# Kernel tuning notes

Hardware: AMD Instinct MI355X
Metric: run time of the kernel (lower is better)

Reference implementation:

```python
import jax, jax.numpy as jnp
import numpy as np

H = 256    # hidden_size
CVQ = 64   # vq_ph_channel
K = 128    # vq_ph_codebook_dim
NL = 5     # num_layers per ConvBlocks
NB = 2     # layers_in_block
KS = 3     # kernel_size


def _ln_c(x, g, b, eps=1e-5):
    # LayerNorm over channel dim of a [B, C, T] tensor
    m = jnp.mean(x, axis=1, keepdims=True)
    v = jnp.mean((x - m) ** 2, axis=1, keepdims=True)
    return (x - m) * jax.lax.rsqrt(v + eps) * g[None, :, None] + b[None, :, None]


def _causal_conv(x, w, b):
    # x [B,Cin,T], w [Cout,Cin,K]; left (causal) padding of K-1
    y = jax.lax.conv_general_dilated(x, w, (1,), [(w.shape[-1] - 1, 0)],
                                     dimension_numbers=('NCH', 'OIH', 'NCH'))
    return y + b[None, :, None]


def _pw(x, w, b):
    # pointwise (kernel-size-1) conv: w [Cout, Cin]
    return jnp.einsum('oi,bit->bot', w, x) + b[None, :, None]


def _conv_blocks(x, mask, ln_g, ln_b, w1, b1, w2, b2, last_g, last_b, post_w, post_b):
    # LeftPadConvBlocks: NL residual blocks x NB sub-blocks of
    # LN -> causal conv (C->2C, k=3) -> *k^-0.5 -> GELU -> 1x1 conv (2C->C), residual + mask
    scale = KS ** -0.5
    for i in range(NL):
        for j in range(NB):
            h = _ln_c(x, ln_g[i, j], ln_b[i, j])
            h = _causal_conv(h, w1[i, j], b1[i, j]) * scale
            h = jax.nn.gelu(h, approximate=False)
            h = _pw(h, w2[i, j], b2[i, j])
            x = (x + h) * mask
    x = _ln_c(x, last_g, last_b) * mask
    x = _causal_conv(x, post_w, post_b) * mask
    return x


def _group_by_segs(h_bct, mel2ph, L):
    # scatter-mean mel frames into phoneme segments; index 0 = padding (dropped)
    h = jnp.swapaxes(h_bct, 1, 2)  # [B, T, H]
    def one(hb, mb):
        s = jnp.zeros((L + 1, hb.shape[-1]), hb.dtype).at[mb].add(hb)
        c = jnp.zeros((L + 1,), hb.dtype).at[mb].add(1.0)
        return s[1:] / jnp.clip(c[1:], 1.0)[:, None]
    g = jax.vmap(one)(h, mel2ph)   # [B, L, H]
    return jnp.swapaxes(g, 1, 2)   # [B, H, L]


def _vq(z, codebook, beta=0.25):
    # EMA-VQ forward math: nearest-codebook lookup + straight-through + commitment loss
    x = jnp.swapaxes(z, 1, 2)                                # [B, T, C]
    d = (jnp.sum(x ** 2, -1, keepdims=True)
         - 2.0 * jnp.einsum('btc,kc->btk', x, codebook)
         + jnp.sum(codebook ** 2, -1))                       # [B, T, K]
    idx = jnp.argmin(d, axis=-1)                             # [B, T]
    q = codebook[idx]                                        # [B, T, C]
    loss = beta * jnp.mean((x - jax.lax.stop_gradient(q)) ** 2)
    q_st = x + jax.lax.stop_gradient(q - x)
    return jnp.swapaxes(q_st, 1, 2), loss, idx


def setup_inputs() -> dict:
    key = jax.random.key(0)
    ks = list(jax.random.split(key, 64))
    it = iter(ks)
    B, T, L = 16, 2048, 512
    f = lambda shape, s: jax.random.normal(next(it), shape, jnp.float32) * s
    inp = {}
    inp['x'] = jax.random.normal(next(it), (B, 80, T), jnp.float32)
    inp['in_nonpadding'] = jnp.ones((B, 1, T), jnp.float32)
    inp['in_mel2ph'] = jnp.sort(jax.random.randint(next(it), (B, T), 1, L + 1), axis=-1)
    inp['ph_nonpadding'] = jnp.ones((B, 1, L), jnp.float32)
    inp['conv_in_w'] = f((H, 80), 0.05)
    inp['conv_in_b'] = jnp.zeros((H,), jnp.float32)
    for p in ('enc', 'pn'):
        inp[p + '_ln_g'] = jnp.ones((NL, NB, H), jnp.float32)
        inp[p + '_ln_b'] = jnp.zeros((NL, NB, H), jnp.float32)
        inp[p + '_w1'] = f((NL, NB, 2 * H, H, KS), 0.03)
        inp[p + '_b1'] = jnp.zeros((NL, NB, 2 * H), jnp.float32)
        inp[p + '_w2'] = f((NL, NB, H, 2 * H), 0.03)
        inp[p + '_b2'] = jnp.zeros((NL, NB, H), jnp.float32)
        inp[p + '_last_g'] = jnp.ones((H,), jnp.float32)
        inp[p + '_last_b'] = jnp.zeros((H,), jnp.float32)
        inp[p + '_post_w'] = f((H, H, KS), 0.03)
        inp[p + '_post_b'] = jnp.zeros((H,), jnp.float32)
    inp['proj_in_w'] = f((CVQ, H), 0.05)
    inp['proj_in_b'] = jnp.zeros((CVQ,), jnp.float32)
    inp['proj_out_w'] = f((H, CVQ), 0.05)
    inp['proj_out_b'] = jnp.zeros((H,), jnp.float32)
    inp['codebook'] = f((K, CVQ), 0.1)
    return inp


def reference(x, in_nonpadding, in_mel2ph, ph_nonpadding,
              conv_in_w, conv_in_b,
              enc_ln_g, enc_ln_b, enc_w1, enc_b1, enc_w2, enc_b2,
              enc_last_g, enc_last_b, enc_post_w, enc_post_b,
              pn_ln_g, pn_ln_b, pn_w1, pn_b1, pn_w2, pn_b2,
              pn_last_g, pn_last_b, pn_post_w, pn_post_b,
              proj_in_w, proj_in_b, proj_out_w, proj_out_b, codebook):
    L = ph_nonpadding.shape[-1]
    h = _pw(x, conv_in_w, conv_in_b) * in_nonpadding                     # ph_conv_in
    h = _conv_blocks(h, in_nonpadding, enc_ln_g, enc_ln_b, enc_w1, enc_b1,
                     enc_w2, enc_b2, enc_last_g, enc_last_b,
                     enc_post_w, enc_post_b) * in_nonpadding             # ph_encoder
    h = _group_by_segs(h, in_mel2ph, L)                                  # [B, H, L]
    h = _conv_blocks(h, ph_nonpadding, pn_ln_g, pn_ln_b, pn_w1, pn_b1,
                     pn_w2, pn_b2, pn_last_g, pn_last_b,
                     pn_post_w, pn_post_b) * ph_nonpadding               # ph_postnet
    z = _pw(h, proj_in_w, proj_in_b)                                     # ph_latents_proj_in
    q, vq_loss, idx = _vq(z, codebook)                                   # VQ
    out = _pw(q, proj_out_w, proj_out_b)                                 # ph_latents_proj_out
    return out, vq_loss, idx
```

## Files before the change

### kernel.cpp

```cpp
#include <hip/hip_runtime.h>
#include <hip/hip_bf16.h>


typedef unsigned short u16;
typedef unsigned int u32;
typedef __attribute__((ext_vector_type(8))) _Float16 f16x8;
typedef __attribute__((ext_vector_type(16))) float f32x16;

#define OUT_LOSS_OFF 2097152
#define OUT_IDX_OFF  2097153

__device__ __forceinline__ void split_f16(float x, u16& h, u16& l) {
    union { _Float16 f; u16 u; } a, b;
    a.f = (_Float16)x;
    float hf = (float)a.f;
    b.f = (_Float16)(x - hf);
    h = a.u; l = b.u;
}

__global__ __launch_bounds__(256) void k_t_mat(const float* __restrict__ w,
                                               float* __restrict__ wt,
                                               int G, int O, int I) {
    size_t n = (size_t)G * O * I;
    for (size_t i = (size_t)blockIdx.x * 256 + threadIdx.x; i < n;
         i += (size_t)gridDim.x * 256) {
        int ci = (int)(i % I);
        int o  = (int)((i / I) % O);
        int g  = (int)(i / ((size_t)I * O));
        wt[((size_t)g * I + ci) * O + o] = w[i];
    }
}

__global__ __launch_bounds__(256) void k_t_w1mf(const float* __restrict__ w,
                                                u16* __restrict__ BH,
                                                u16* __restrict__ BL, int S) {
    size_t N = (size_t)S * 3 * 16 * 16 * 64 * 8;
    for (size_t i = (size_t)blockIdx.x * 256 + threadIdx.x; i < N;
         i += (size_t)gridDim.x * 256) {
        int j = (int)(i & 7); size_t r = i >> 3;
        int L = (int)(r & 63); r >>= 6;
        int nt = (int)(r & 15); r >>= 4;
        int kb = (int)(r & 15); r >>= 4;
        int k3 = (int)(r % 3); int s = (int)(r / 3);
        int oc = nt * 32 + (L & 31);
        int c = kb * 16 + ((L >> 5) << 3) + j;
        float v = w[(((size_t)s * 512 + oc) * 256 + c) * 3 + k3];
        u16 h, l; split_f16(v, h, l);
        BH[i] = h; BL[i] = l;
    }
}

__global__ __launch_bounds__(256) void k_t_w2mf(const float* __restrict__ w,
                                                u16* __restrict__ BH,
                                                u16* __restrict__ BL, int S) {
    size_t N = (size_t)S * 32 * 8 * 64 * 8;
    for (size_t i = (size_t)blockIdx.x * 256 + threadIdx.x; i < N;
         i += (size_t)gridDim.x * 256) {
        int j = (int)(i & 7);
        int L = (int)((i >> 3) & 63);
        int nt = (int)((i >> 9) & 7);
        int kb = (int)((i >> 12) & 31);
        int s = (int)(i >> 17);
        int oc = nt * 32 + (L & 31);
        int ic = kb * 16 + ((L >> 5) << 3) + j;
        float v = w[((size_t)s * 256 + oc) * 512 + ic];
        u16 h, l; split_f16(v, h, l);
        BH[i] = h; BL[i] = l;
    }
}

__global__ __launch_bounds__(256) void k_t_wpmf(const float* __restrict__ w,
                                                u16* __restrict__ BH,
                                                u16* __restrict__ BL) {
    int i = blockIdx.x * 256 + threadIdx.x;
    int j = i & 7;
    int L = (i >> 3) & 63;
    int nt = (i >> 9) & 7;
    int kb = (i >> 12) & 15;
    int k3 = i >> 16;
    int oc = nt * 32 + (L & 31);
    int c = kb * 16 + ((L >> 5) << 3) + j;
    float v = w[((size_t)oc * 256 + c) * 3 + k3];
    u16 h, l; split_f16(v, h, l);
    BH[i] = h; BL[i] = l;
}

template <int CIN, int COUT, int CHUNK, bool STATS>
__global__ __launch_bounds__(256) void k_pw(const float* __restrict__ x,
                                            const float* __restrict__ wt,
                                            const float* __restrict__ bias,
                                            const float* __restrict__ mask,
                                            float* __restrict__ y,
                                            float* __restrict__ MM,
                                            float* __restrict__ IV, int T) {
    extern __shared__ float X[];
    constexpr int NG = COUT / CHUNK;
    __shared__ float rs[64 * NG], rs2[64 * NG];
    const int b = blockIdx.y, t0 = blockIdx.x * 64;
    for (int i = threadIdx.x; i < CIN * 64; i += 256) {
        int ci = i >> 6, j = i & 63;
        X[i] = x[((size_t)b * CIN + ci) * T + t0 + j];
    }
    __syncthreads();
    const int tl = threadIdx.x & 63;
    const int g = __builtin_amdgcn_readfirstlane((int)(threadIdx.x >> 6));
    float acc[CHUNK];
#pragma unroll
    for (int o = 0; o < CHUNK; o++) acc[o] = 0.f;
    for (int i = 0; i < CIN; i++) {
        float xv = X[i * 64 + tl];
        const float* wr = wt + (size_t)i * COUT + g * CHUNK;
#pragma unroll
        for (int o = 0; o < CHUNK; o++) acc[o] = fmaf(wr[o], xv, acc[o]);
    }
    float mk = mask ? mask[(size_t)b * T + t0 + tl] : 1.0f;
    float s = 0.f, s2 = 0.f;
#pragma unroll
    for (int o = 0; o < CHUNK; o++) {
        int oc = g * CHUNK + o;
        float val = (acc[o] + bias[oc]) * mk;
        y[((size_t)b * COUT + oc) * T + t0 + tl] = val;
        s += val; s2 += val * val;
    }
    if constexpr (STATS) {
        rs[g * 64 + tl] = s; rs2[g * 64 + tl] = s2;
        __syncthreads();
        if (threadIdx.x < 64) {
            float ss = 0.f, ss2 = 0.f;
#pragma unroll
            for (int gg = 0; gg < NG; gg++) {
                ss += rs[gg * 64 + threadIdx.x];
                ss2 += rs2[gg * 64 + threadIdx.x];
            }
            float m = ss * (1.0f / COUT);
            float var = ss2 * (1.0f / COUT) - m * m;
            MM[(size_t)b * T + t0 + threadIdx.x] = m;
            IV[(size_t)b * T + t0 + threadIdx.x] = 1.0f / sqrtf(var + 1e-5f);
        }
    }
}

__global__ __launch_bounds__(512, 6) void k_sub(
    const float* __restrict__ xin, float* __restrict__ xout,
    const float* __restrict__ MMi, const float* __restrict__ IVi,
    const float* __restrict__ lng, const float* __restrict__ lnb,
    const u16* __restrict__ B1H, const u16* __restrict__ B1L,
    const float* __restrict__ b1,
    const u16* __restrict__ B2H, const u16* __restrict__ B2L,
    const float* __restrict__ b2, const float* __restrict__ mask,
    float* __restrict__ MMo, float* __restrict__ IVo, int T) {
    __shared__ __align__(16) char smem[40128];
    u16* LH = (u16*)smem;
    u16* LL = (u16*)(smem + 17952);
    u16* GH = (u16*)smem;
    u16* GL = (u16*)(smem + 17952);
    float* SOUT = (float*)smem;
    float* rs  = (float*)(smem + 36032);
    float* rs2 = (float*)(smem + 38080);

    const int tid = threadIdx.x;
    const int b = blockIdx.y, t0 = blockIdx.x * 32;
    const size_t xoff = (size_t)b * 256 * T;
    const size_t bT = (size_t)b * T;

    {
        int jj = tid & 31;
        int cg = tid >> 5;
        int t = t0 - 2 + jj;
        bool ok = (t >= 0);
        float m = ok ? MMi[bT + t] : 0.f;
        float v = ok ? IVi[bT + t] : 0.f;
#pragma unroll
        for (int i = 0; i < 16; i++) {
            int c = cg + i * 16;
            float xv = ok ? xin[xoff + (size_t)c * T + t] : 0.f;
            float ln = ok ? ((xv - m) * v * lng[c] + lnb[c]) : 0.f;
            u16 h, l; split_f16(ln, h, l);
            LH[jj * 264 + c] = h; LL[jj * 264 + c] = l;
        }
        int j2 = 32 + (tid >> 8);
        int c2 = tid & 255;
        int t2 = t0 + 30 + (tid >> 8);
        float m2 = MMi[bT + t2], v2 = IVi[bT + t2];
        float x2 = xin[xoff + (size_t)c2 * T + t2];
        float ln2 = (x2 - m2) * v2 * lng[c2] + lnb[c2];
        u16 h2, l2; split_f16(ln2, h2, l2);
        LH[j2 * 264 + c2] = h2; LL[j2 * 264 + c2] = l2;
    }
    __syncthreads();

    const int lane = tid & 63;
    const int w = tid >> 6;
    const int arow = lane & 31;
    const int acol = (lane >> 5) << 3;
    const int thalf = (lane >> 5) << 2;
    const float ks = 0.5773502691896258f;
    const int oc_l = w * 32 + (lane & 31);
    const u16* b1h0 = B1H + (size_t)w * 512 + (size_t)lane * 8;
    const u16* b1l0 = B1L + (size_t)w * 512 + (size_t)lane * 8;
    const u16* b1h1 = B1H + (size_t)(8 + w) * 512 + (size_t)lane * 8;
    const u16* b1l1 = B1L + (size_t)(8 + w) * 512 + (size_t)lane * 8;
    const u16* b2h = B2H + (size_t)w * 512 + (size_t)lane * 8;
    const u16* b2l = B2L + (size_t)w * 512 + (size_t)lane * 8;
    const int grow = (lane & 31) * 264;

    f32x16 c0, c1;
#pragma unroll
    for (int r = 0; r < 16; r++) { c0[r] = 0.f; c1[r] = 0.f; }
    __builtin_amdgcn_s_setprio(1);
#pragma unroll 4
    for (int kk = 0; kk < 48; kk++) {
        int k3 = kk >> 4, kb = kk & 15;
        int ao = (arow + k3) * 264 + kb * 16 + acol;
        f16x8 ah = *(const f16x8*)&LH[ao];
        f16x8 al = *(const f16x8*)&LL[ao];
        f16x8 bh0 = *(const f16x8*)(b1h0 + (size_t)kk * 8192);
        f16x8 bl0 = *(const f16x8*)(b1l0 + (size_t)kk * 8192);
        f16x8 bh1 = *(const f16x8*)(b1h1 + (size_t)kk * 8192);
        f16x8 bl1 = *(const f16x8*)(b1l1 + (size_t)kk * 8192);
        c0 = __builtin_amdgcn_mfma_f32_32x32x16_f16(ah, bh0, c0, 0, 0, 0);
        c1 = __builtin_amdgcn_mfma_f32_32x32x16_f16(ah, bh1, c1, 0, 0, 0);
        c0 = __builtin_amdgcn_mfma_f32_32x32x16_f16(ah, bl0, c0, 0, 0, 0);
        c1 = __builtin_amdgcn_mfma_f32_32x32x16_f16(ah, bl1, c1, 0, 0, 0);
        c0 = __builtin_amdgcn_mfma_f32_32x32x16_f16(al, bh0, c0, 0, 0, 0);
        c1 = __builtin_amdgcn_mfma_f32_32x32x16_f16(al, bh1, c1, 0, 0, 0);
    }
    __builtin_amdgcn_s_setprio(0);
    __syncthreads();

    {
        float bb = b1[oc_l];
#pragma unroll
        for (int r = 0; r < 16; r++) {
            int trow = thalf + ((r >> 2) << 3) + (r & 3);
            float y = (c0[r] + bb) * ks;
            float ge = 0.5f * y * (1.0f + erff(y * 0.7071067811865476f));
            u16 h, l; split_f16(ge, h, l);
            GH[trow * 264 + oc_l] = h; GL[trow * 264 + oc_l] = l;
        }
    }
    __syncthreads();

    f32x16 c2acc;
#pragma unroll
    for (int r = 0; r < 16; r++) c2acc[r] = 0.f;
    __builtin_amdgcn_s_setprio(1);
#pragma unroll 4
    for (int i = 0; i < 16; i++) {
        f16x8 gh = *(const f16x8*)&GH[grow + i * 16 + acol];
        f16x8 gl = *(const f16x8*)&GL[grow + i * 16 + acol];
        f16x8 bh2 = *(const f16x8*)(b2h + (size_t)i * 4096);
        f16x8 bl2 = *(const f16x8*)(b2l + (size_t)i * 4096);
        c2acc = __builtin_amdgcn_mfma_f32_32x32x16_f16(gh, bh2, c2acc, 0, 0, 0);
        c2acc = __builtin_amdgcn_mfma_f32_32x32x16_f16(gh, bl2, c2acc, 0, 0, 0);
        c2acc = __builtin_amdgcn_mfma_f32_32x32x16_f16(gl, bh2, c2acc, 0, 0, 0);
    }
    __builtin_amdgcn_s_setprio(0);
    __syncthreads();

    {
        float bb = b1[256 + oc_l];
#pragma unroll
        for (int r = 0; r < 16; r++) {
            int trow = thalf + ((r >> 2) << 3) + (r & 3);
            float y = (c1[r] + bb) * ks;
            float ge = 0.5f * y * (1.0f + erff(y * 0.7071067811865476f));
            u16 h, l; split_f16(ge, h, l);
            GH[trow * 264 + oc_l] = h; GL[trow * 264 + oc_l] = l;
        }
    }
    __syncthreads();

    __builtin_amdgcn_s_setprio(1);
#pragma unroll 4
    for (int i = 0; i < 16; i++) {
        f16x8 gh = *(const f16x8*)&GH[grow + i * 16 + acol];
        f16x8 gl = *(const f16x8*)&GL[grow + i * 16 + acol];
        f16x8 bh2 = *(const f16x8*)(b2h + (size_t)(16 + i) * 4096);
        f16x8 bl2 = *(const f16x8*)(b2l + (size_t)(16 + i) * 4096);
        c2acc = __builtin_amdgcn_mfma_f32_32x32x16_f16(gh, bh2, c2acc, 0, 0, 0);
        c2acc = __builtin_amdgcn_mfma_f32_32x32x16_f16(gh, bl2, c2acc, 0, 0, 0);
        c2acc = __builtin_amdgcn_mfma_f32_32x32x16_f16(gl, bh2, c2acc, 0, 0, 0);
    }
    __builtin_amdgcn_s_setprio(0);
    __syncthreads();

#pragma unroll
    for (int r = 0; r < 16; r++) {
        int trow = thalf + ((r >> 2) << 3) + (r & 3);
        SOUT[trow * 260 + oc_l] = c2acc[r];
    }
    __syncthreads();
    {
        int t = tid & 31, cg = tid >> 5;
        float mk = mask[bT + t0 + t];
        float s = 0.f, s2 = 0.f;
#pragma unroll
        for (int i = 0; i < 16; i++) {
            int c = cg * 16 + i;
            size_t adr = xoff + (size_t)c * T + t0 + t;
            float val = (xin[adr] + SOUT[t * 260 + c] + b2[c]) * mk;
            xout[adr] = val;
            s += val; s2 += val * val;
        }
        rs[tid] = s; rs2[tid] = s2;
    }
    __syncthreads();
    if (tid < 32) {
        float ss = 0.f, ss2 = 0.f;
#pragma unroll
        for (int k = 0; k < 16; k++) {
            ss += rs[k * 32 + tid]; ss2 += rs2[k * 32 + tid];
        }
        float m = ss * (1.0f / 256.0f);
        float var = ss2 * (1.0f / 256.0f) - m * m;
        MMo[bT + t0 + tid] = m;
        IVo[bT + t0 + tid] = 1.0f / sqrtf(var + 1e-5f);
    }
}

__global__ __launch_bounds__(512, 8) void k_lnc(
    const float* __restrict__ xin, float* __restrict__ xout,
    const float* __restrict__ MM, const float* __restrict__ IV,
    const float* __restrict__ lg, const float* __restrict__ lb,
    const u16* __restrict__ BH, const u16* __restrict__ BL,
    const float* __restrict__ bias, const float* __restrict__ mask, int T) {
    __shared__ __align__(16) char smem[35904];
    u16* LH = (u16*)smem;
    u16* LL = (u16*)(smem + 17952);
    float* SOUT = (float*)smem;

    const int tid = threadIdx.x;
    const int b = blockIdx.y, t0 = blockIdx.x * 32;
    const size_t xoff = (size_t)b * 256 * T;
    const size_t bT = (size_t)b * T;

    {
        int jj = tid & 31;
        int cg = tid >> 5;
        int t = t0 - 2 + jj;
        bool ok = (t >= 0);
        float m = ok ? MM[bT + t] : 0.f;
        float v = ok ? IV[bT + t] : 0.f;
        float mk = ok ? mask[bT + t] : 0.f;
#pragma unroll
        for (int i = 0; i < 16; i++) {
            int c = cg + i * 16;
            float xv = ok ? xin[xoff + (size_t)c * T + t] : 0.f;
            float ln = ok ? ((xv - m) * v * lg[c] + lb[c]) * mk : 0.f;
            u16 h, l; split_f16(ln, h, l);
            LH[jj * 264 + c] = h; LL[jj * 264 + c] = l;
        }
        int j2 = 32 + (tid >> 8);
        int c2 = tid & 255;
        int t2 = t0 + 30 + (tid >> 8);
        float ln2 = ((xin[xoff + (size_t)c2 * T + t2] - MM[bT + t2]) *
                     IV[bT + t2] * lg[c2] + lb[c2]) * mask[bT + t2];
        u16 h2, l2; split_f16(ln2, h2, l2);
        LH[j2 * 264 + c2] = h2; LL[j2 * 264 + c2] = l2;
    }
    __syncthreads();

    const int lane = tid & 63;
    const int w = tid >> 6;
    const int arow = lane & 31;
    const int acol = (lane >> 5) << 3;
    const int thalf = (lane >> 5) << 2;
    const u16* bph = BH + (size_t)w * 512 + (size_t)lane * 8;
    const u16* bpl = BL + (size_t)w * 512 + (size_t)lane * 8;

    f32x16 aH, aM;
#pragma unroll
    for (int r = 0; r < 16; r++) { aH[r] = 0.f; aM[r] = 0.f; }
    __builtin_amdgcn_s_setprio(1);
#pragma unroll 4
    for (int kk = 0; kk < 48; kk++) {
        int k3 = kk >> 4, kb = kk & 15;
        int ao = (arow + k3) * 264 + kb * 16 + acol;
        f16x8 ah = *(const f16x8*)&LH[ao];
        f16x8 al = *(const f16x8*)&LL[ao];
        f16x8 bh = *(const f16x8*)(bph + (size_t)kk * 4096);
        f16x8 bl = *(const f16x8*)(bpl + (size_t)kk * 4096);
        aH = __builtin_amdgcn_mfma_f32_32x32x16_f16(ah, bh, aH, 0, 0, 0);
        aM = __builtin_amdgcn_mfma_f32_32x32x16_f16(ah, bl, aM, 0, 0, 0);
        aM = __builtin_amdgcn_mfma_f32_32x32x16_f16(al, bh, aM, 0, 0, 0);
    }
    __builtin_amdgcn_s_setprio(0);
    __syncthreads();
    {
        int oc = w * 32 + (lane & 31);
#pragma unroll
        for (int r = 0; r < 16; r++) {
            int trow = thalf + ((r >> 2) << 3) + (r & 3);
            SOUT[trow * 260 + oc] = aH[r] + aM[r];
        }
    }
    __syncthreads();
    {
        int t = tid & 31, cg = tid >> 5;
        float mk = mask[bT + t0 + t];
#pragma unroll
        for (int i = 0; i < 16; i++) {
            int c = cg * 16 + i;
            xout[xoff + (size_t)c * T + t0 + t] =
                (SOUT[t * 260 + c] + bias[c]) * mk;
        }
    }
}

__global__ __launch_bounds__(256) void k_counts(const int* __restrict__ m2p,
                                                int* __restrict__ cnt) {
    __shared__ int c[512];
    int b = blockIdx.x;
    for (int i = threadIdx.x; i < 512; i += 256) c[i] = 0;
    __syncthreads();
    for (int t = threadIdx.x; t < 2048; t += 256) {
        int p = m2p[b * 2048 + t];
        if (p >= 1 && p <= 512) atomicAdd(&c[p - 1], 1);
    }
    __syncthreads();
    for (int i = threadIdx.x; i < 512; i += 256) cnt[b * 512 + i] = c[i];
}

__global__ __launch_bounds__(256) void k_scatter(const float* __restrict__ h,
                                                 const int* __restrict__ m2p,
                                                 float* __restrict__ g) {
    extern __shared__ float sm[];
    float* HT = sm;
    int* ph = (int*)(sm + 256 * 65);
    int b = blockIdx.y, t0 = blockIdx.x * 64;
    if (threadIdx.x < 64) ph[threadIdx.x] = m2p[b * 2048 + t0 + threadIdx.x];
    for (int i = threadIdx.x; i < 256 * 64; i += 256) {
        int c = i >> 6, j = i & 63;
        HT[c * 65 + j] = h[((size_t)b * 256 + c) * 2048 + t0 + j];
    }
    __syncthreads();
    int c = threadIdx.x;
    float run = 0.f;
    int cur = ph[0];
    for (int j = 0; j < 64; j++) {
        int p = ph[j];
        if (p != cur) {
            if (cur >= 1 && cur <= 512)
                atomicAdd(&g[((size_t)b * 256 + c) * 512 + cur - 1], run);
            run = 0.f;
            cur = p;
        }
        run += HT[c * 65 + j];
    }
    if (cur >= 1 && cur <= 512)
        atomicAdd(&g[((size_t)b * 256 + c) * 512 + cur - 1], run);
}

__global__ __launch_bounds__(512) void k_postprep(float* __restrict__ g,
                                                  const int* __restrict__ cnt,
                                                  float* __restrict__ MM,
                                                  float* __restrict__ IV) {
    int b = blockIdx.x, l = threadIdx.x;
    int c1 = cnt[b * 512 + l];
    if (c1 < 1) c1 = 1;
    float rc = 1.0f / (float)c1;
    float s = 0.f, s2 = 0.f;
    for (int c = 0; c < 256; c++) {
        size_t idx = ((size_t)b * 256 + c) * 512 + l;
        float v = g[idx] * rc;
        g[idx] = v;
        s += v; s2 += v * v;
    }
    float m = s * (1.0f / 256.0f);
    float var = s2 * (1.0f / 256.0f) - m * m;
    MM[(size_t)b * 512 + l] = m;
    IV[(size_t)b * 512 + l] = 1.0f / sqrtf(var + 1e-5f);
}

__global__ __launch_bounds__(256) void k_vq(const float* __restrict__ z,
                                            const float* __restrict__ cb,
                                            int* __restrict__ idxout,
                                            float* __restrict__ out,
                                            float* __restrict__ lossacc) {
    int n = blockIdx.x * 256 + threadIdx.x;
    int b = n >> 9, l = n & 511;
    float zr[64];
#pragma unroll
    for (int c = 0; c < 64; c++) zr[c] = z[((size_t)b * 64 + c) * 512 + l];
    float best = 3.4e38f;
    int bi = 0;
    for (int k = 0; k < 128; k++) {
        const float* cr = cb + k * 64;
        float d = 0.f;
#pragma unroll
        for (int c = 0; c < 64; c++) {
            float t = zr[c] - cr[c];
            d = fmaf(t, t, d);
        }
        if (d < best) { best = d; bi = k; }
    }
    idxout[n] = bi;
    out[OUT_IDX_OFF + n] = (float)bi;
    atomicAdd(lossacc, best);
}

__global__ void k_loss(const float* __restrict__ acc, float* __restrict__ out) {
    if (threadIdx.x == 0 && blockIdx.x == 0)
        out[OUT_LOSS_OFF] = 0.25f * acc[0] * (1.0f / 524288.0f);
}

__global__ __launch_bounds__(256) void k_projout(const float* __restrict__ cb,
                                                 const int* __restrict__ idx,
                                                 const float* __restrict__ wt,
                                                 const float* __restrict__ bias,
                                                 float* __restrict__ out) {
    __shared__ float Q[64 * 64];
    __shared__ int ids[64];
    int b = blockIdx.y, l0 = blockIdx.x * 64;
    if (threadIdx.x < 64) ids[threadIdx.x] = idx[b * 512 + l0 + threadIdx.x];
    __syncthreads();
    for (int i = threadIdx.x; i < 4096; i += 256) {
        int c = i >> 6, l = i & 63;
        Q[c * 64 + l] = cb[ids[l] * 64 + c];
    }
    __syncthreads();
    int tl = threadIdx.x & 63;
    int g = __builtin_amdgcn_readfirstlane((int)(threadIdx.x >> 6));
    float acc[64];
#pragma unroll
    for (int o = 0; o < 64; o++) acc[o] = 0.f;
    for (int i = 0; i < 64; i++) {
        float xv = Q[i * 64 + tl];
        const float* wr = wt + i * 256 + g * 64;
#pragma unroll
        for (int o = 0; o < 64; o++) acc[o] = fmaf(wr[o], xv, acc[o]);
    }
#pragma unroll
    for (int o = 0; o < 64; o++) {
        int oc = g * 64 + o;
        out[(size_t)b * 131072 + (size_t)oc * 512 + l0 + tl] = acc[o] + bias[oc];
    }
}

extern "C" void kernel_launch(void* const* d_in, const int* in_sizes, int n_in,
                              void* d_out, int out_size, void* d_ws, size_t ws_size,
                              hipStream_t stream) {
    (void)in_sizes; (void)n_in; (void)out_size; (void)ws_size;
    const float* x          = (const float*)d_in[0];
    const float* in_np      = (const float*)d_in[1];
    const int*   mel2ph     = (const int*)d_in[2];
    const float* ph_np      = (const float*)d_in[3];
    const float* conv_in_w  = (const float*)d_in[4];
    const float* conv_in_b  = (const float*)d_in[5];
    const float* e_ln_g = (const float*)d_in[6];
    const float* e_ln_b = (const float*)d_in[7];
    const float* e_w1   = (const float*)d_in[8];
    const float* e_b1   = (const float*)d_in[9];
    const float* e_w2   = (const float*)d_in[10];
    const float* e_b2   = (const float*)d_in[11];
    const float* e_lg   = (const float*)d_in[12];
    const float* e_lb   = (const float*)d_in[13];
    const float* e_pw   = (const float*)d_in[14];
    const float* e_pb   = (const float*)d_in[15];
    const float* p_ln_g = (const float*)d_in[16];
    const float* p_ln_b = (const float*)d_in[17];
    const float* p_w1   = (const float*)d_in[18];
    const float* p_b1   = (const float*)d_in[19];
    const float* p_w2   = (const float*)d_in[20];
    const float* p_b2   = (const float*)d_in[21];
    const float* p_lg   = (const float*)d_in[22];
    const float* p_lb   = (const float*)d_in[23];
    const float* p_pw   = (const float*)d_in[24];
    const float* p_pb   = (const float*)d_in[25];
    const float* proj_in_w  = (const float*)d_in[26];
    const float* proj_in_b  = (const float*)d_in[27];
    const float* proj_out_w = (const float*)d_in[28];
    const float* proj_out_b = (const float*)d_in[29];
    const float* codebook   = (const float*)d_in[30];
    float* out = (float*)d_out;

    float* ws = (float*)d_ws;
    float* A      = ws;
    float* Bb     = A + 8388608;
    float* CINT   = Bb + 8388608;
    float* PINT   = CINT + 20480;
    float* POUTT  = PINT + 16384;
    float* Z      = POUTT + 16384;
    float* MM0    = Z + 524288;
    float* IV0    = MM0 + 32768;
    float* MM1    = IV0 + 32768;
    float* IV1    = MM1 + 32768;
    int*   CNT    = (int*)(IV1 + 32768);
    int*   IDX    = CNT + 8192;
    float* LOSS   = (float*)(IDX + 8192);
    u16*   BH1E   = (u16*)(LOSS + 64);
    u16*   BL1E   = BH1E + 3932160;
    u16*   BH1P   = BL1E + 3932160;
    u16*   BL1P   = BH1P + 3932160;
    u16*   BH2E   = BL1P + 3932160;
    u16*   BL2E   = BH2E + 1310720;
    u16*   BH2P   = BL2E + 1310720;
    u16*   BL2P   = BH2P + 1310720;
    u16*   PH_E   = BL2P + 1310720;
    u16*   PL_E   = PH_E + 196608;
    u16*   PH_P   = PL_E + 196608;
    u16*   PL_P   = PH_P + 196608;

    k_t_w1mf<<<dim3(4096), dim3(256), 0, stream>>>(e_w1, BH1E, BL1E, 10);
    k_t_w1mf<<<dim3(4096), dim3(256), 0, stream>>>(p_w1, BH1P, BL1P, 10);
    k_t_w2mf<<<dim3(2048), dim3(256), 0, stream>>>(e_w2, BH2E, BL2E, 10);
    k_t_w2mf<<<dim3(2048), dim3(256), 0, stream>>>(p_w2, BH2P, BL2P, 10);
    k_t_wpmf<<<dim3(768),  dim3(256), 0, stream>>>(e_pw, PH_E, PL_E);
    k_t_wpmf<<<dim3(768),  dim3(256), 0, stream>>>(p_pw, PH_P, PL_P);
    k_t_mat  <<<dim3(80),  dim3(256), 0, stream>>>(conv_in_w, CINT, 1, 256, 80);
    k_t_mat  <<<dim3(64),  dim3(256), 0, stream>>>(proj_in_w, PINT, 1, 64, 256);
    k_t_mat  <<<dim3(64),  dim3(256), 0, stream>>>(proj_out_w, POUTT, 1, 256, 64);

    const size_t sm_scat = 256 * 65 * sizeof(float) + 64 * sizeof(int);

    k_pw<80, 256, 64, true><<<dim3(32, 16), dim3(256), 80 * 64 * 4, stream>>>(
        x, CINT, conv_in_b, in_np, A, MM0, IV0, 2048);

    float* cur = A;
    float* nxt = Bb;
    for (int s = 0; s < 10; s++) {
        float* mi = (s & 1) ? MM1 : MM0;
        float* vi = (s & 1) ? IV1 : IV0;
        float* mo = (s & 1) ? MM0 : MM1;
        float* vo = (s & 1) ? IV0 : IV1;
        k_sub<<<dim3(64, 16), dim3(512), 0, stream>>>(
            cur, nxt, mi, vi, e_ln_g + s * 256, e_ln_b + s * 256,
            BH1E + (size_t)s * 393216, BL1E + (size_t)s * 393216, e_b1 + s * 512,
            BH2E + (size_t)s * 131072, BL2E + (size_t)s * 131072, e_b2 + s * 256,
            in_np, mo, vo, 2048);
        float* t = cur; cur = nxt; nxt = t;
    }
    k_lnc<<<dim3(64, 16), dim3(512), 0, stream>>>(
        cur, nxt, MM0, IV0, e_lg, e_lb, PH_E, PL_E, e_pb, in_np, 2048);

    hipMemsetAsync(A, 0, (size_t)2097152 * 4, stream);
    hipMemsetAsync(LOSS, 0, 4, stream);
    k_counts<<<dim3(16), dim3(256), 0, stream>>>(mel2ph, CNT);
    k_scatter<<<dim3(32, 16), dim3(256), sm_scat, stream>>>(Bb, mel2ph, A);
    k_postprep<<<dim3(16), dim3(512), 0, stream>>>(A, CNT, MM0, IV0);

    cur = A; nxt = Bb;
    for (int s = 0; s < 10; s++) {
        float* mi = (s & 1) ? MM1 : MM0;
        float* vi = (s & 1) ? IV1 : IV0;
        float* mo = (s & 1) ? MM0 : MM1;
        float* vo = (s & 1) ? IV0 : IV1;
        k_sub<<<dim3(16, 16), dim3(512), 0, stream>>>(
            cur, nxt, mi, vi, p_ln_g + s * 256, p_ln_b + s * 256,
            BH1P + (size_t)s * 393216, BL1P + (size_t)s * 393216, p_b1 + s * 512,
            BH2P + (size_t)s * 131072, BL2P + (size_t)s * 131072, p_b2 + s * 256,
            ph_np, mo, vo, 512);
        float* t = cur; cur = nxt; nxt = t;
    }
    k_lnc<<<dim3(16, 16), dim3(512), 0, stream>>>(
        cur, nxt, MM0, IV0, p_lg, p_lb, PH_P, PL_P, p_pb, ph_np, 512);

    k_pw<256, 64, 16, false><<<dim3(8, 16), dim3(256), 256 * 64 * 4, stream>>>(
        Bb, PINT, proj_in_b, nullptr, Z, nullptr, nullptr, 512);

    k_vq<<<dim3(32), dim3(256), 0, stream>>>(Z, codebook, IDX, out, LOSS);
    k_loss<<<dim3(1), dim3(64), 0, stream>>>(LOSS, out);
    k_projout<<<dim3(8, 16), dim3(256), 0, stream>>>(codebook, IDX, POUTT,
                                                     proj_out_b, out);
}
```

Before: 2.416 ms.

## Template conv sub-block kernels on time tile and use 64-frame tiles for encoder

```diff
diff --git a/kernel.cpp b/kernel.cpp
--- a/kernel.cpp
+++ b/kernel.cpp
@@ -140,7 +140,8 @@
     }
 }
 
-__global__ __launch_bounds__(512, 6) void k_sub(
+template <int M>
+__global__ __launch_bounds__(512, (M == 32 ? 6 : 4)) void k_sub(
     const float* __restrict__ xin, float* __restrict__ xout,
     const float* __restrict__ MMi, const float* __restrict__ IVi,
     const float* __restrict__ lng, const float* __restrict__ lnb,
@@ -149,38 +150,42 @@
     const u16* __restrict__ B2H, const u16* __restrict__ B2L,
     const float* __restrict__ b2, const float* __restrict__ mask,
     float* __restrict__ MMo, float* __restrict__ IVo, int T) {
-    __shared__ __align__(16) char smem[40128];
+    constexpr int MT = M / 32;
+    constexpr int SH = (M + 2) * 264 * 2;
+    constexpr int CG = 512 / M;
+    constexpr int CPT = 256 / CG;
+    __shared__ __align__(16) char smem[2 * SH + 4096];
     u16* LH = (u16*)smem;
-    u16* LL = (u16*)(smem + 17952);
+    u16* LL = (u16*)(smem + SH);
     u16* GH = (u16*)smem;
-    u16* GL = (u16*)(smem + 17952);
+    u16* GL = (u16*)(smem + SH);
     float* SOUT = (float*)smem;
-    float* rs  = (float*)(smem + 36032);
-    float* rs2 = (float*)(smem + 38080);
+    float* rs  = (float*)(smem + 2 * SH);
+    float* rs2 = (float*)(smem + 2 * SH + 2048);
 
     const int tid = threadIdx.x;
-    const int b = blockIdx.y, t0 = blockIdx.x * 32;
+    const int b = blockIdx.y, t0 = blockIdx.x * M;
     const size_t xoff = (size_t)b * 256 * T;
     const size_t bT = (size_t)b * T;
 
     {
-        int jj = tid & 31;
-        int cg = tid >> 5;
+        int jj = tid & (M - 1);
+        int cg = tid / M;
         int t = t0 - 2 + jj;
         bool ok = (t >= 0);
         float m = ok ? MMi[bT + t] : 0.f;
         float v = ok ? IVi[bT + t] : 0.f;
 #pragma unroll
-        for (int i = 0; i < 16; i++) {
-            int c = cg + i * 16;
+        for (int i = 0; i < CPT; i++) {
+            int c = cg + i * CG;
             float xv = ok ? xin[xoff + (size_t)c * T + t] : 0.f;
             float ln = ok ? ((xv - m) * v * lng[c] + lnb[c]) : 0.f;
             u16 h, l; split_f16(ln, h, l);
             LH[jj * 264 + c] = h; LL[jj * 264 + c] = l;
         }
-        int j2 = 32 + (tid >> 8);
+        int j2 = M + (tid >> 8);
         int c2 = tid & 255;
-        int t2 = t0 + 30 + (tid >> 8);
+        int t2 = t0 + (M - 2) + (tid >> 8);
         float m2 = MMi[bT + t2], v2 = IVi[bT + t2];
         float x2 = xin[xoff + (size_t)c2 * T + t2];
         float ln2 = (x2 - m2) * v2 * lng[c2] + lnb[c2];
@@ -202,28 +207,32 @@
     const u16* b1l1 = B1L + (size_t)(8 + w) * 512 + (size_t)lane * 8;
     const u16* b2h = B2H + (size_t)w * 512 + (size_t)lane * 8;
     const u16* b2l = B2L + (size_t)w * 512 + (size_t)lane * 8;
-    const int grow = (lane & 31) * 264;
-
-    f32x16 c0, c1;
-#pragma unroll
-    for (int r = 0; r < 16; r++) { c0[r] = 0.f; c1[r] = 0.f; }
+
+    f32x16 c0[MT], c1[MT];
+#pragma unroll
+    for (int m = 0; m < MT; m++)
+#pragma unroll
+        for (int r = 0; r < 16; r++) { c0[m][r] = 0.f; c1[m][r] = 0.f; }
     __builtin_amdgcn_s_setprio(1);
-#pragma unroll 4
+#pragma unroll 2
     for (int kk = 0; kk < 48; kk++) {
         int k3 = kk >> 4, kb = kk & 15;
-        int ao = (arow + k3) * 264 + kb * 16 + acol;
-        f16x8 ah = *(const f16x8*)&LH[ao];
-        f16x8 al = *(const f16x8*)&LL[ao];
         f16x8 bh0 = *(const f16x8*)(b1h0 + (size_t)kk * 8192);
         f16x8 bl0 = *(const f16x8*)(b1l0 + (size_t)kk * 8192);
         f16x8 bh1 = *(const f16x8*)(b1h1 + (size_t)kk * 8192);
         f16x8 bl1 = *(const f16x8*)(b1l1 + (size_t)kk * 8192);
-        c0 = __builtin_amdgcn_mfma_f32_32x32x16_f16(ah, bh0, c0, 0, 0, 0);
-        c1 = __builtin_amdgcn_mfma_f32_32x32x16_f16(ah, bh1, c1, 0, 0, 0);
-        c0 = __builtin_amdgcn_mfma_f32_32x32x16_f16(ah, bl0, c0, 0, 0, 0);
-        c1 = __builtin_amdgcn_mfma_f32_32x32x16_f16(ah, bl1, c1, 0, 0, 0);
-        c0 = __builtin_amdgcn_mfma_f32_32x32x16_f16(al, bh0, c0, 0, 0, 0);
-        c1 = __builtin_amdgcn_mfma_f32_32x32x16_f16(al, bh1, c1, 0, 0, 0);
+#pragma unroll
+        for (int m = 0; m < MT; m++) {
+            int ao = (m * 32 + arow + k3) * 264 + kb * 16 + acol;
+            f16x8 ah = *(const f16x8*)&LH[ao];
+            f16x8 al = *(const f16x8*)&LL[ao];
+            c0[m] = __builtin_amdgcn_mfma_f32_32x32x16_f16(ah, bh0, c0[m], 0, 0, 0);
+            c1[m] = __builtin_amdgcn_mfma_f32_32x32x16_f16(ah, bh1, c1[m], 0, 0, 0);
+            c0[m] = __builtin_amdgcn_mfma_f32_32x32x16_f16(ah, bl0, c0[m], 0, 0, 0);
+            c1[m] = __builtin_amdgcn_mfma_f32_32x32x16_f16(ah, bl1, c1[m], 0, 0, 0);
+            c0[m] = __builtin_amdgcn_mfma_f32_32x32x16_f16(al, bh0, c0[m], 0, 0, 0);
+            c1[m] = __builtin_amdgcn_mfma_f32_32x32x16_f16(al, bh1, c1[m], 0, 0, 0);
+        }
     }
     __builtin_amdgcn_s_setprio(0);
     __syncthreads();
@@ -231,29 +240,37 @@
     {
         float bb = b1[oc_l];
 #pragma unroll
-        for (int r = 0; r < 16; r++) {
-            int trow = thalf + ((r >> 2) << 3) + (r & 3);
-            float y = (c0[r] + bb) * ks;
-            float ge = 0.5f * y * (1.0f + erff(y * 0.7071067811865476f));
-            u16 h, l; split_f16(ge, h, l);
-            GH[trow * 264 + oc_l] = h; GL[trow * 264 + oc_l] = l;
-        }
-    }
-    __syncthreads();
-
-    f32x16 c2acc;
-#pragma unroll
-    for (int r = 0; r < 16; r++) c2acc[r] = 0.f;
+        for (int m = 0; m < MT; m++)
+#pragma unroll
+            for (int r = 0; r < 16; r++) {
+                int trow = m * 32 + thalf + ((r >> 2) << 3) + (r & 3);
+                float y = (c0[m][r] + bb) * ks;
+                float ge = 0.5f * y * (1.0f + erff(y * 0.7071067811865476f));
+                u16 h, l; split_f16(ge, h, l);
+                GH[trow * 264 + oc_l] = h; GL[trow * 264 + oc_l] = l;
+            }
+    }
+    __syncthreads();
+
+    f32x16 c2acc[MT];
+#pragma unroll
+    for (int m = 0; m < MT; m++)
+#pragma unroll
+        for (int r = 0; r < 16; r++) c2acc[m][r] = 0.f;
     __builtin_amdgcn_s_setprio(1);
-#pragma unroll 4
+#pragma unroll 2
     for (int i = 0; i < 16; i++) {
-        f16x8 gh = *(const f16x8*)&GH[grow + i * 16 + acol];
-        f16x8 gl = *(const f16x8*)&GL[grow + i * 16 + acol];
         f16x8 bh2 = *(const f16x8*)(b2h + (size_t)i * 4096);
         f16x8 bl2 = *(const f16x8*)(b2l + (size_t)i * 4096);
-        c2acc = __builtin_amdgcn_mfma_f32_32x32x16_f16(gh, bh2, c2acc, 0, 0, 0);
-        c2acc = __builtin_amdgcn_mfma_f32_32x32x16_f16(gh, bl2, c2acc, 0, 0, 0);
-        c2acc = __builtin_amdgcn_mfma_f32_32x32x16_f16(gl, bh2, c2acc, 0, 0, 0);
+#pragma unroll
+        for (int m = 0; m < MT; m++) {
+            int go = (m * 32 + arow) * 264 + i * 16 + acol;
+            f16x8 gh = *(const f16x8*)&GH[go];
+            f16x8 gl = *(const f16x8*)&GL[go];
+            c2acc[m] = __builtin_amdgcn_mfma_f32_32x32x16_f16(gh, bh2, c2acc[m], 0, 0, 0);
+            c2acc[m] = __builtin_amdgcn_mfma_f32_32x32x16_f16(gh, bl2, c2acc[m], 0, 0, 0);
+            c2acc[m] = __builtin_amdgcn_mfma_f32_32x32x16_f16(gl, bh2, c2acc[m], 0, 0, 0);
+        }
     }
     __builtin_amdgcn_s_setprio(0);
     __syncthreads();
@@ -261,43 +278,51 @@
     {
         float bb = b1[256 + oc_l];
 #pragma unroll
-        for (int r = 0; r < 16; r++) {
-            int trow = thalf + ((r >> 2) << 3) + (r & 3);
-            float y = (c1[r] + bb) * ks;
-            float ge = 0.5f * y * (1.0f + erff(y * 0.7071067811865476f));
-            u16 h, l; split_f16(ge, h, l);
-            GH[trow * 264 + oc_l] = h; GL[trow * 264 + oc_l] = l;
-        }
+        for (int m = 0; m < MT; m++)
+#pragma unroll
+            for (int r = 0; r < 16; r++) {
+                int trow = m * 32 + thalf + ((r >> 2) << 3) + (r & 3);
+                float y = (c1[m][r] + bb) * ks;
+                float ge = 0.5f * y * (1.0f + erff(y * 0.7071067811865476f));
+                u16 h, l; split_f16(ge, h, l);
+                GH[trow * 264 + oc_l] = h; GL[trow * 264 + oc_l] = l;
+            }
     }
     __syncthreads();
 
     __builtin_amdgcn_s_setprio(1);
-#pragma unroll 4
+#pragma unroll 2
     for (int i = 0; i < 16; i++) {
-        f16x8 gh = *(const f16x8*)&GH[grow + i * 16 + acol];
-        f16x8 gl = *(const f16x8*)&GL[grow + i * 16 + acol];
         f16x8 bh2 = *(const f16x8*)(b2h + (size_t)(16 + i) * 4096);
         f16x8 bl2 = *(const f16x8*)(b2l + (size_t)(16 + i) * 4096);
-        c2acc = __builtin_amdgcn_mfma_f32_32x32x16_f16(gh, bh2, c2acc, 0, 0, 0);
-        c2acc = __builtin_amdgcn_mfma_f32_32x32x16_f16(gh, bl2, c2acc, 0, 0, 0);
-        c2acc = __builtin_amdgcn_mfma_f32_32x32x16_f16(gl, bh2, c2acc, 0, 0, 0);
+#pragma unroll
+        for (int m = 0; m < MT; m++) {
+            int go = (m * 32 + arow) * 264 + i * 16 + acol;
+            f16x8 gh = *(const f16x8*)&GH[go];
+            f16x8 gl = *(const f16x8*)&GL[go];
+            c2acc[m] = __builtin_amdgcn_mfma_f32_32x32x16_f16(gh, bh2, c2acc[m], 0, 0, 0);
+            c2acc[m] = __builtin_amdgcn_mfma_f32_32x32x16_f16(gh, bl2, c2acc[m], 0, 0, 0);
+            c2acc[m] = __builtin_amdgcn_mfma_f32_32x32x16_f16(gl, bh2, c2acc[m], 0, 0, 0);
+        }
     }
     __builtin_amdgcn_s_setprio(0);
     __syncthreads();
 
 #pragma unroll
-    for (int r = 0; r < 16; r++) {
-        int trow = thalf + ((r >> 2) << 3) + (r & 3);
-        SOUT[trow * 260 + oc_l] = c2acc[r];
-    }
+    for (int m = 0; m < MT; m++)
+#pragma unroll
+        for (int r = 0; r < 16; r++) {
+            int trow = m * 32 + thalf + ((r >> 2) << 3) + (r & 3);
+            SOUT[trow * 260 + oc_l] = c2acc[m][r];
+        }
     __syncthreads();
     {
-        int t = tid & 31, cg = tid >> 5;
+        int t = tid & (M - 1), cg = tid / M;
         float mk = mask[bT + t0 + t];
         float s = 0.f, s2 = 0.f;
 #pragma unroll
-        for (int i = 0; i < 16; i++) {
-            int c = cg * 16 + i;
+        for (int i = 0; i < CPT; i++) {
+            int c = cg * CPT + i;
             size_t adr = xoff + (size_t)c * T + t0 + t;
             float val = (xin[adr] + SOUT[t * 260 + c] + b2[c]) * mk;
             xout[adr] = val;
@@ -306,11 +331,11 @@
         rs[tid] = s; rs2[tid] = s2;
     }
     __syncthreads();
-    if (tid < 32) {
+    if (tid < M) {
         float ss = 0.f, ss2 = 0.f;
 #pragma unroll
-        for (int k = 0; k < 16; k++) {
-            ss += rs[k * 32 + tid]; ss2 += rs2[k * 32 + tid];
+        for (int k = 0; k < CG; k++) {
+            ss += rs[k * M + tid]; ss2 += rs2[k * M + tid];
         }
         float m = ss * (1.0f / 256.0f);
         float var = ss2 * (1.0f / 256.0f) - m * m;
@@ -319,41 +344,46 @@
     }
 }
 
-__global__ __launch_bounds__(512, 8) void k_lnc(
+template <int M>
+__global__ __launch_bounds__(512, (M == 32 ? 8 : 4)) void k_lnc(
     const float* __restrict__ xin, float* __restrict__ xout,
     const float* __restrict__ MM, const float* __restrict__ IV,
     const float* __restrict__ lg, const float* __restrict__ lb,
     const u16* __restrict__ BH, const u16* __restrict__ BL,
     const float* __restrict__ bias, const float* __restrict__ mask, int T) {
-    __shared__ __align__(16) char smem[35904];
+    constexpr int MT = M / 32;
+    constexpr int SH = (M + 2) * 264 * 2;
+    constexpr int CG = 512 / M;
+    constexpr int CPT = 256 / CG;
+    __shared__ __align__(16) char smem[2 * SH];
     u16* LH = (u16*)smem;
-    u16* LL = (u16*)(smem + 17952);
+    u16* LL = (u16*)(smem + SH);
     float* SOUT = (float*)smem;
 
     const int tid = threadIdx.x;
-    const int b = blockIdx.y, t0 = blockIdx.x * 32;
+    const int b = blockIdx.y, t0 = blockIdx.x * M;
     const size_t xoff = (size_t)b * 256 * T;
     const size_t bT = (size_t)b * T;
 
     {
-        int jj = tid & 31;
-        int cg = tid >> 5;
+        int jj = tid & (M - 1);
+        int cg = tid / M;
         int t = t0 - 2 + jj;
         bool ok = (t >= 0);
         float m = ok ? MM[bT + t] : 0.f;
         float v = ok ? IV[bT + t] : 0.f;
         float mk = ok ? mask[bT + t] : 0.f;
 #pragma unroll
-        for (int i = 0; i < 16; i++) {
-            int c = cg + i * 16;
+        for (int i = 0; i < CPT; i++) {
+            int c = cg + i * CG;
             float xv = ok ? xin[xoff + (size_t)c * T + t] : 0.f;
             float ln = ok ? ((xv - m) * v * lg[c] + lb[c]) * mk : 0.f;
             u16 h, l; split_f16(ln, h, l);
             LH[jj * 264 + c] = h; LL[jj * 264 + c] = l;
         }
-        int j2 = 32 + (tid >> 8);
+        int j2 = M + (tid >> 8);
         int c2 = tid & 255;
-        int t2 = t0 + 30 + (tid >> 8);
+        int t2 = t0 + (M - 2) + (tid >> 8);
         float ln2 = ((xin[xoff + (size_t)c2 * T + t2] - MM[bT + t2]) *
                      IV[bT + t2] * lg[c2] + lb[c2]) * mask[bT + t2];
         u16 h2, l2; split_f16(ln2, h2, l2);
@@ -369,39 +399,46 @@
     const u16* bph = BH + (size_t)w * 512 + (size_t)lane * 8;
     const u16* bpl = BL + (size_t)w * 512 + (size_t)lane * 8;
 
-    f32x16 aH, aM;
-#pragma unroll
-    for (int r = 0; r < 16; r++) { aH[r] = 0.f; aM[r] = 0.f; }
+    f32x16 aH[MT], aM[MT];
+#pragma unroll
+    for (int m = 0; m < MT; m++)
+#pragma unroll
+        for (int r = 0; r < 16; r++) { aH[m][r] = 0.f; aM[m][r] = 0.f; }
     __builtin_amdgcn_s_setprio(1);
-#pragma unroll 4
+#pragma unroll 2
     for (int kk = 0; kk < 48; kk++) {
         int k3 = kk >> 4, kb = kk & 15;
-        int ao = (arow + k3) * 264 + kb * 16 + acol;
-        f16x8 ah = *(const f16x8*)&LH[ao];
-        f16x8 al = *(const f16x8*)&LL[ao];
         f16x8 bh = *(const f16x8*)(bph + (size_t)kk * 4096);
         f16x8 bl = *(const f16x8*)(bpl + (size_t)kk * 4096);
-        aH = __builtin_amdgcn_mfma_f32_32x32x16_f16(ah, bh, aH, 0, 0, 0);
-        aM = __builtin_amdgcn_mfma_f32_32x32x16_f16(ah, bl, aM, 0, 0, 0);
-        aM = __builtin_amdgcn_mfma_f32_32x32x16_f16(al, bh, aM, 0, 0, 0);
+#pragma unroll
+        for (int m = 0; m < MT; m++) {
+            int ao = (m * 32 + arow + k3) * 264 + kb * 16 + acol;
+            f16x8 ah = *(const f16x8*)&LH[ao];
+            f16x8 al = *(const f16x8*)&LL[ao];
+            aH[m] = __builtin_amdgcn_mfma_f32_32x32x16_f16(ah, bh, aH[m], 0, 0, 0);
+            aM[m] = __builtin_amdgcn_mfma_f32_32x32x16_f16(ah, bl, aM[m], 0, 0, 0);
+            aM[m] = __builtin_amdgcn_mfma_f32_32x32x16_f16(al, bh, aM[m], 0, 0, 0);
+        }
     }
     __builtin_amdgcn_s_setprio(0);
     __syncthreads();
     {
         int oc = w * 32 + (lane & 31);
 #pragma unroll
-        for (int r = 0; r < 16; r++) {
-            int trow = thalf + ((r >> 2) << 3) + (r & 3);
-            SOUT[trow * 260 + oc] = aH[r] + aM[r];
-        }
+        for (int m = 0; m < MT; m++)
+#pragma unroll
+            for (int r = 0; r < 16; r++) {
+                int trow = m * 32 + thalf + ((r >> 2) << 3) + (r & 3);
+                SOUT[trow * 260 + oc] = aH[m][r] + aM[m][r];
+            }
     }
     __syncthreads();
     {
-        int t = tid & 31, cg = tid >> 5;
+        int t = tid & (M - 1), cg = tid / M;
         float mk = mask[bT + t0 + t];
 #pragma unroll
-        for (int i = 0; i < 16; i++) {
-            int c = cg * 16 + i;
+        for (int i = 0; i < CPT; i++) {
+            int c = cg * CPT + i;
             xout[xoff + (size_t)c * T + t0 + t] =
                 (SOUT[t * 260 + c] + bias[c]) * mk;
         }
@@ -624,14 +661,14 @@
         float* vi = (s & 1) ? IV1 : IV0;
         float* mo = (s & 1) ? MM0 : MM1;
         float* vo = (s & 1) ? IV0 : IV1;
-        k_sub<<<dim3(64, 16), dim3(512), 0, stream>>>(
+        k_sub<64><<<dim3(32, 16), dim3(512), 0, stream>>>(
             cur, nxt, mi, vi, e_ln_g + s * 256, e_ln_b + s * 256,
             BH1E + (size_t)s * 393216, BL1E + (size_t)s * 393216, e_b1 + s * 512,
             BH2E + (size_t)s * 131072, BL2E + (size_t)s * 131072, e_b2 + s * 256,
             in_np, mo, vo, 2048);
         float* t = cur; cur = nxt; nxt = t;
     }
-    k_lnc<<<dim3(64, 16), dim3(512), 0, stream>>>(
+    k_lnc<64><<<dim3(32, 16), dim3(512), 0, stream>>>(
         cur, nxt, MM0, IV0, e_lg, e_lb, PH_E, PL_E, e_pb, in_np, 2048);
 
     hipMemsetAsync(A, 0, (size_t)2097152 * 4, stream);
@@ -646,14 +683,14 @@
         float* vi = (s & 1) ? IV1 : IV0;
         float* mo = (s & 1) ? MM0 : MM1;
         float* vo = (s & 1) ? IV0 : IV1;
-        k_sub<<<dim3(16, 16), dim3(512), 0, stream>>>(
+        k_sub<32><<<dim3(16, 16), dim3(512), 0, stream>>>(
             cur, nxt, mi, vi, p_ln_g + s * 256, p_ln_b + s * 256,
             BH1P + (size_t)s * 393216, BL1P + (size_t)s * 393216, p_b1 + s * 512,
             BH2P + (size_t)s * 131072, BL2P + (size_t)s * 131072, p_b2 + s * 256,
             ph_np, mo, vo, 512);
         float* t = cur; cur = nxt; nxt = t;
     }
-    k_lnc<<<dim3(16, 16), dim3(512), 0, stream>>>(
+    k_lnc<32><<<dim3(16, 16), dim3(512), 0, stream>>>(
         cur, nxt, MM0, IV0, p_lg, p_lb, PH_P, PL_P, p_pb, ph_np, 512);
 
     k_pw<256, 64, 16, false><<<dim3(8, 16), dim3(256), 256 * 64 * 4, stream>>>(
```

Measured after the change: 2.274 ms. 1.06x faster.
